# Performance work log

Hardware: AMD Instinct MI355X
Metric: run time of the kernel (lower is better)

Reference implementation:

```python
import jax, jax.numpy as jnp
import numpy as np

LN_EPS = 1e-5

def _layernorm(z, g, b):
    m = jnp.mean(z, axis=-1, keepdims=True)
    v = jnp.mean(jnp.square(z - m), axis=-1, keepdims=True)
    return (z - m) / jnp.sqrt(v + LN_EPS) * g + b

def setup_inputs() -> dict:
    key = jax.random.key(0)
    ks = jax.random.split(key, 8)
    B, N, C, H = 16, 1024, 384, 6
    Dff = 4 * C
    s = 0.02
    return {
        "x": jax.random.normal(ks[0], (B, N, C), dtype=jnp.float32),
        "ln1_g": jnp.ones((C,), jnp.float32),
        "ln1_b": jnp.zeros((C,), jnp.float32),
        "qkv_w": jax.random.normal(ks[1], (3 * C, C), jnp.float32) * s,
        "proj_w": jax.random.normal(ks[2], (C, C), jnp.float32) * s,
        "proj_b": jnp.zeros((C,), jnp.float32),
        "gate_h": jnp.ones((H,), jnp.float32),
        "ln2_g": jnp.ones((C,), jnp.float32),
        "ln2_b": jnp.zeros((C,), jnp.float32),
        "fc1_w": jax.random.normal(ks[3], (Dff, C), jnp.float32) * s,
        "fc1_b": jnp.zeros((Dff,), jnp.float32),
        "fc2_w": jax.random.normal(ks[4], (C, Dff), jnp.float32) * s,
        "fc2_b": jnp.zeros((C,), jnp.float32),
        "gate_mlp": jnp.ones((Dff,), jnp.float32),
    }

def reference(x, ln1_g, ln1_b, qkv_w, proj_w, proj_b, gate_h,
              ln2_g, ln2_b, fc1_w, fc1_b, fc2_w, fc2_b, gate_mlp):
    B, N, C = x.shape
    H = gate_h.shape[0]
    Dh = C // H
    scale = Dh ** -0.5

    # Attention branch
    h = _layernorm(x, ln1_g, ln1_b)
    qkv = (h @ qkv_w.T).reshape(B, N, 3, H, Dh).transpose(2, 0, 3, 1, 4)  # [3,B,H,N,Dh]
    q, k, v = qkv[0], qkv[1], qkv[2]
    attn = jax.nn.softmax(jnp.einsum('bhnd,bhmd->bhnm', q, k) * scale, axis=-1)  # [B,H,N,N]
    o = jnp.einsum('bhnm,bhmd->bhnd', attn, v)            # [B,H,N,Dh]
    o = o.transpose(0, 2, 1, 3) * gate_h[None, None, :, None]  # per-head gate
    o = o.reshape(B, N, C) @ proj_w.T + proj_b
    x = x + o

    # MLP branch (exact GELU, per-neuron gate)
    h2 = _layernorm(x, ln2_g, ln2_b)
    m = jax.nn.gelu(h2 @ fc1_w.T + fc1_b, approximate=False) * gate_mlp
    x = x + (m @ fc2_w.T + fc2_b)
    return x
```

## Files before the change

kernel.cpp:

```cpp
#include <hip/hip_runtime.h>
#include <hip/hip_bf16.h>
#include <cstdint>
#include <cstddef>

#define B_   16
#define N_   1024
#define C_   384
#define H_   6
#define DFF_ 1536
#define R_   16384

typedef __attribute__((ext_vector_type(8))) __bf16 bf16x8;
typedef __attribute__((ext_vector_type(4))) float  f32x4;
typedef __attribute__((ext_vector_type(8))) unsigned short u16x8;
typedef __attribute__((ext_vector_type(4))) unsigned short u16x4;

__device__ __forceinline__ float bf2f(unsigned short u){
    unsigned int x = ((unsigned int)u) << 16;
    return __builtin_bit_cast(float, x);
}
__device__ __forceinline__ unsigned short f2bf(float f){
    return __builtin_bit_cast(unsigned short, __float2bfloat16(f));
}
__device__ __forceinline__ unsigned int cvt_pk_bf16(float a, float b){
    unsigned int r;
    asm("v_cvt_pk_bf16_f32 %0, %1, %2" : "=v"(r) : "v"(a), "v"(b));
    return r;
}
__device__ __forceinline__ float fast_exp2(float x){
    float r;
    asm("v_exp_f32 %0, %1" : "=v"(r) : "v"(x));
    return r;
}
__device__ __forceinline__ void gload16(const void* g, void* l){
    __builtin_amdgcn_global_load_lds(
        (const __attribute__((address_space(1))) unsigned int*)g,
        (__attribute__((address_space(3))) unsigned int*)l, 16, 0, 0);
}
__device__ __forceinline__ float gelu_f(float u){
    float z  = fabsf(u) * 0.70710678118654752f;
    float t  = __builtin_amdgcn_rcpf(1.0f + 0.47047f*z);
    float e  = __expf(-z*z);
    float p  = t*(0.3480242f + t*(-0.0958798f + t*0.7478556f));
    float er = 1.0f - p*e;
    return 0.5f*u*(1.0f + copysignf(er, u));
}
__device__ __forceinline__ float ldv(const float* p, size_t i){ return p[i]; }
__device__ __forceinline__ float ldv(const __hip_bfloat16* p, size_t i){ return __bfloat162float(p[i]); }

__global__ __launch_bounds__(256) void ln1_cvt_kernel(
    const float* __restrict__ x, const float* __restrict__ g,
    const float* __restrict__ b, __hip_bfloat16* __restrict__ out,
    const float* __restrict__ i0, __hip_bfloat16* __restrict__ o0, int n0,
    const float* __restrict__ i1, __hip_bfloat16* __restrict__ o1, int n1,
    const float* __restrict__ i2, __hip_bfloat16* __restrict__ o2, int n2,
    const float* __restrict__ i3, __hip_bfloat16* __restrict__ o3, int n3)
{
    if (blockIdx.x < 4096){
        const int lane = threadIdx.x & 63;
        const int wave = threadIdx.x >> 6;
        const int row  = blockIdx.x*4 + wave;
        const float* xr = x + (size_t)row*C_;
        float v[6];
        float s = 0.f;
        #pragma unroll
        for (int i=0;i<6;i++){ v[i] = xr[lane + i*64]; s += v[i]; }
        #pragma unroll
        for (int m=1;m<64;m<<=1) s += __shfl_xor(s, m);
        const float mean = s * (1.0f/C_);
        float sq = 0.f;
        #pragma unroll
        for (int i=0;i<6;i++){ float d = v[i]-mean; sq += d*d; }
        #pragma unroll
        for (int m=1;m<64;m<<=1) sq += __shfl_xor(sq, m);
        const float rstd = rsqrtf(sq*(1.0f/C_) + 1e-5f);
        #pragma unroll
        for (int i=0;i<6;i++){
            int c = lane + i*64;
            out[(size_t)row*C_ + c] = __float2bfloat16((v[i]-mean)*rstd*g[c] + b[c]);
        }
    } else {
        const int total = n0+n1+n2+n3;
        for (int i = (blockIdx.x-4096)*blockDim.x + threadIdx.x; i < total; i += 1024*blockDim.x){
            int k = i;
            if (k < n0){ o0[k] = __float2bfloat16(i0[k]); continue; }
            k -= n0;
            if (k < n1){ o1[k] = __float2bfloat16(i1[k]); continue; }
            k -= n1;
            if (k < n2){ o2[k] = __float2bfloat16(i2[k]); continue; }
            k -= n2;
            o3[k] = __float2bfloat16(i3[k]);
        }
    }
}

template<typename T>
__global__ __launch_bounds__(256) void ln_kernel(
    const T* __restrict__ x, const float* __restrict__ g,
    const float* __restrict__ b, __hip_bfloat16* __restrict__ out)
{
    const int lane = threadIdx.x & 63;
    const int wave = threadIdx.x >> 6;
    const int row  = blockIdx.x*4 + wave;
    const T* xr = x + (size_t)row*C_;
    float v[6];
    float s = 0.f;
    #pragma unroll
    for (int i=0;i<6;i++){ v[i] = ldv(xr, lane + i*64); s += v[i]; }
    #pragma unroll
    for (int m=1;m<64;m<<=1) s += __shfl_xor(s, m);
    const float mean = s * (1.0f/C_);
    float sq = 0.f;
    #pragma unroll
    for (int i=0;i<6;i++){ float d = v[i]-mean; sq += d*d; }
    #pragma unroll
    for (int m=1;m<64;m<<=1) sq += __shfl_xor(sq, m);
    const float rstd = rsqrtf(sq*(1.0f/C_) + 1e-5f);
    #pragma unroll
    for (int i=0;i<6;i++){
        int c = lane + i*64;
        out[(size_t)row*C_ + c] = __float2bfloat16((v[i]-mean)*rstd*g[c] + b[c]);
    }
}

#define BK2 32
enum { EPI_QKV=0, EPI_PROJ=1, EPI_FC1=2, EPI_FC2=3 };

template<int EPI, int BMt, int BNt, int NBUF, int MW, int NTH>
__global__ __launch_bounds__(NTH, MW) void gemm_bt(
    const __hip_bfloat16* __restrict__ A,
    const __hip_bfloat16* __restrict__ W,
    const int M, const int N, const int K,
    const float* __restrict__ bias,
    const float* __restrict__ resid,
    const __hip_bfloat16* __restrict__ residb,
    const float* __restrict__ gate,
    float* __restrict__ outf,
    __hip_bfloat16* __restrict__ outb)
{
    constexpr int NWAVE = NTH/64;
    constexpr int NWC   = (BNt >= 128) ? 2 : 1;
    constexpr int NWR   = NWAVE/NWC;
    constexpr int WRS   = BMt/NWR;
    constexpr int MI    = WRS/16;
    constexpr int APASS = (BMt*BK2*2)/(NTH*16);
    constexpr int BPASS = (BNt*BK2*2)/(NTH*16);
    constexpr int RPP   = NTH/4;
    __shared__ __align__(16) unsigned short As[NBUF][BMt*BK2];
    __shared__ __align__(16) unsigned short Bs[NBUF][BNt*BK2];
    const int t = threadIdx.x;
    const int l = t & 63;
    const int w = t >> 6;
    const int wr = (NWC==2) ? (w >> 1) : w;
    const int wc = (NWC==2) ? (w & 1)  : 0;
    const int nb = N / BNt;
    const int rbX = (M/BMt) >> 3;
    const int X  = blockIdx.x & 7;
    const int j8 = blockIdx.x >> 3;
    const int rb = X*rbX + j8 / nb;
    const int cb = j8 % nb;
    const int srow2 = t >> 2;
    const int sgcol = (((t&3) - ((t>>3)&3)) & 3) * 8;
    f32x4 acc[MI][4];
    #pragma unroll
    for (int i=0;i<MI;i++)
        #pragma unroll
        for (int jj=0;jj<4;jj++) acc[i][jj] = (f32x4){0.f,0.f,0.f,0.f};

    const size_t arow0 = (size_t)rb*BMt + srow2;
    const size_t brow0 = (size_t)cb*BNt + srow2;

    auto STAGE = [&](int buf, int k0){
        #pragma unroll
        for (int c=0;c<APASS;c++)
            gload16(A + (arow0 + c*RPP)*K + k0 + sgcol, (char*)&As[buf][0] + c*(NTH*16) + t*16);
        #pragma unroll
        for (int c=0;c<BPASS;c++)
            gload16(W + (brow0 + c*RPP)*K + k0 + sgcol, (char*)&Bs[buf][0] + c*(NTH*16) + t*16);
    };

    auto COMPUTE = [&](int buf){
        const char* as = (const char*)&As[buf][0];
        const char* bs = (const char*)&Bs[buf][0];
        bf16x8 af[MI], bw[4];
        #pragma unroll
        for (int i=0;i<MI;i++){
            const int r = wr*WRS + i*16 + (l&15);
            const int sl = ((l>>4) + ((r>>1)&3)) & 3;
            af[i] = *(const bf16x8*)(as + r*64 + sl*16);
        }
        #pragma unroll
        for (int i=0;i<4;i++){
            const int r = wc*64 + i*16 + (l&15);
            const int sl = ((l>>4) + ((r>>1)&3)) & 3;
            bw[i] = *(const bf16x8*)(bs + r*64 + sl*16);
        }
        #pragma unroll
        for (int mi=0;mi<MI;mi++)
            #pragma unroll
            for (int ni=0;ni<4;ni++)
                acc[mi][ni] = __builtin_amdgcn_mfma_f32_16x16x32_bf16(af[mi], bw[ni], acc[mi][ni], 0,0,0);
    };

    const int nst = K/BK2;
    if constexpr (NBUF==2){
        STAGE(0, 0);
        for (int s=0; s<nst; ++s){
            asm volatile("s_waitcnt vmcnt(0)" ::: "memory");
            __builtin_amdgcn_s_barrier();
            asm volatile("" ::: "memory");
            if (s+1 < nst) STAGE((s+1)&1, (s+1)*BK2);
            COMPUTE(s&1);
        }
    } else {
        STAGE(0, 0);
        STAGE(1, BK2);
        int cur = 0, stb = 2;
        for (int s=0; s<nst; ++s){
            if (s < nst-1){
                if constexpr (APASS+BPASS==4) asm volatile("s_waitcnt vmcnt(4)" ::: "memory");
                else                          asm volatile("s_waitcnt vmcnt(3)" ::: "memory");
            } else {
                asm volatile("s_waitcnt vmcnt(0)" ::: "memory");
            }
            __builtin_amdgcn_s_barrier();
            asm volatile("" ::: "memory");
            if (s+2 < nst){
                STAGE(stb, (s+2)*BK2);
                stb = (stb+1==3) ? 0 : stb+1;
            }
            COMPUTE(cur);
            cur = (cur+1==3) ? 0 : cur+1;
        }
    }
    const int rowBase = rb*BMt + wr*WRS;
    const int colBase = cb*BNt + wc*64;
    if constexpr (EPI==EPI_QKV){
        unsigned short* ob = (unsigned short*)outb;
        #pragma unroll
        for (int ni=0; ni<4; ni++){
            const int col = colBase + ni*16 + (l&15);
            const int p = col/384, rem = col - p*384;
            const int hh = rem>>6, d = rem&63;
            #pragma unroll
            for (int mi=0; mi<MI; mi++){
                const int row0 = rowBase + mi*16 + (l>>4)*4;
                const int bb = row0>>10, n = row0&1023;
                if (p==2){
                    u16x4 pk;
                    #pragma unroll
                    for (int jj=0;jj<4;jj++) pk[jj] = f2bf(acc[mi][ni][jj]);
                    *(u16x4*)(ob + (size_t)2*6291456 + ((size_t)(bb*H_+hh)*64 + d)*1024 + n) = pk;
                } else {
                    #pragma unroll
                    for (int jj=0;jj<4;jj++)
                        ob[(((size_t)((p*16+bb)*6+hh))<<16) + ((size_t)(n+jj)<<6) + d] = f2bf(acc[mi][ni][jj]);
                }
            }
        }
    } else {
        #pragma unroll
        for (int ni=0; ni<4; ni++){
            const int col = colBase + ni*16 + (l&15);
            #pragma unroll
            for (int mi=0; mi<MI; mi++){
                #pragma unroll
                for (int jj=0;jj<4;jj++){
                    const int row = rowBase + mi*16 + (l>>4)*4 + jj;
                    const float vx = acc[mi][ni][jj];
                    size_t idx = (size_t)row*N + col;
                    if constexpr (EPI==EPI_PROJ){
                        outb[idx] = __float2bfloat16(resid[idx] + vx + bias[col]);
                    } else if constexpr (EPI==EPI_FC2){
                        outf[idx] = bf2f(*((const unsigned short*)residb + idx)) + vx + bias[col];
                    } else {
                        outb[idx] = __float2bfloat16(gelu_f(vx + bias[col]) * gate[col]);
                    }
                }
            }
        }
    }
}

__global__ __launch_bounds__(256) void attn_mfma(
    const __hip_bfloat16* __restrict__ qg,
    const __hip_bfloat16* __restrict__ kg,
    const __hip_bfloat16* __restrict__ vtg,
    const float* __restrict__ gate_h,
    __hip_bfloat16* __restrict__ og)
{
    __shared__ __align__(16) unsigned short Ks [3][64*64];
    __shared__ __align__(16) unsigned short Vts[3][64*64];
    const int t = threadIdx.x;
    const int l = t & 63;
    const int w = t >> 6;
    const int X  = blockIdx.x & 7;
    const int j8 = blockIdx.x >> 3;
    const int bh = X*12 + (j8 >> 3);
    const int n0 = (j8 & 7) * 128;
    const int h  = bh % H_;
    const int b  = bh / H_;
    const unsigned short* qp  = (const unsigned short*)qg  + ((size_t)bh*N_ + n0 + w*32)*64;
    const unsigned short* kp  = (const unsigned short*)kg  + (size_t)bh*N_*64;
    const unsigned short* vtp = (const unsigned short*)vtg + (size_t)bh*64*N_;

    bf16x8 qf[2][2];
    #pragma unroll
    for (int mt=0;mt<2;mt++)
        #pragma unroll
        for (int dc=0;dc<2;dc++){
            u16x8 raw = *(const u16x8*)(qp + ((size_t)(mt*16 + (l&15)))*64 + dc*32 + (l>>4)*8);
            u16x8 sc;
            #pragma unroll
            for (int j=0;j<8;j++) sc[j] = f2bf(bf2f(raw[j]) * 0.1803368801111244f);
            qf[mt][dc] = __builtin_bit_cast(bf16x8, sc);
        }

    int qk_off[4][2], pv_off[2][4];
    #pragma unroll
    for (int t4=0;t4<4;t4++){
        const int i    = l & 15;
        const int row  = 8*(i>>2) + (i&3) + 4*(t4&1) + 32*(t4>>1);
        const int swzr = (row&3) | (((row>>3)&1)<<2);
        #pragma unroll
        for (int dc=0;dc<2;dc++)
            qk_off[t4][dc] = row*128 + ((dc*64 + (l>>4)*16) ^ (swzr<<4));
    }
    #pragma unroll
    for (int nt=0;nt<4;nt++){
        const int row  = nt*16 + (l&15);
        const int swzr = (row&3) | (((row>>3)&1)<<2);
        #pragma unroll
        for (int kc=0;kc<2;kc++)
            pv_off[kc][nt] = row*128 + ((kc*64 + (l>>4)*16) ^ (swzr<<4));
    }

    const int sr  = t >> 3;
    const int sce = (t & 7) * 8;

    auto STAGE = [&](int buf, int kt){
        #pragma unroll
        for (int c=0;c<2;c++){
            const int r    = sr + c*32;
            const int swzr = (r&3) | (((r>>3)&1)<<2);
            const int col  = sce ^ (swzr<<3);
            gload16(kp  + ((size_t)(kt*64 + r))*64 + col, (char*)&Ks [buf][0] + (c*256 + t)*16);
            gload16(vtp + (size_t)r*N_ + kt*64 + col,     (char*)&Vts[buf][0] + (c*256 + t)*16);
        }
    };

    f32x4 o_acc[2][4];
    #pragma unroll
    for (int i=0;i<2;i++)
        #pragma unroll
        for (int jj=0;jj<4;jj++) o_acc[i][jj] = (f32x4){0.f,0.f,0.f,0.f};
    float rs_part[2] = {0.f, 0.f};

    STAGE(0, 0);
    STAGE(1, 1);
    int cur = 0, stb = 2;
    for (int kt=0; kt<16; kt++){
        if (kt < 15) asm volatile("s_waitcnt vmcnt(4)" ::: "memory");
        else         asm volatile("s_waitcnt vmcnt(0)" ::: "memory");
        __builtin_amdgcn_s_barrier();
        asm volatile("" ::: "memory");
        if (kt < 14){
            STAGE(stb, kt+2);
            stb = (stb+1==3) ? 0 : stb+1;
        }
        const char* ks = (const char*)&Ks[cur][0];
        const char* vs = (const char*)&Vts[cur][0];

        f32x4 s_acc[4][2];
        #pragma unroll
        for (int i=0;i<4;i++)
            #pragma unroll
            for (int jj=0;jj<2;jj++) s_acc[i][jj] = (f32x4){0.f,0.f,0.f,0.f};
        #pragma unroll
        for (int t4=0;t4<4;t4++)
            #pragma unroll
            for (int dc=0;dc<2;dc++){
                bf16x8 kf = *(const bf16x8*)(ks + qk_off[t4][dc]);
                #pragma unroll
                for (int mt=0;mt<2;mt++)
                    s_acc[t4][mt] = __builtin_amdgcn_mfma_f32_16x16x32_bf16(kf, qf[mt][dc], s_acc[t4][mt], 0,0,0);
            }
        #pragma unroll
        for (int mt=0;mt<2;mt++){
            float acc_s = 0.f;
            #pragma unroll
            for (int t4=0;t4<4;t4++){
                #pragma unroll
                for (int jj=0;jj<4;jj++){
                    float e = fast_exp2(s_acc[t4][mt][jj]);
                    s_acc[t4][mt][jj] = e;
                    acc_s += e;
                }
            }
            rs_part[mt] += acc_s;
        }
        #pragma unroll
        for (int kc=0;kc<2;kc++){
            union { unsigned int u[4]; bf16x8 v; } pu[2];
            #pragma unroll
            for (int mt=0;mt<2;mt++){
                pu[mt].u[0] = cvt_pk_bf16(s_acc[2*kc  ][mt][0], s_acc[2*kc  ][mt][1]);
                pu[mt].u[1] = cvt_pk_bf16(s_acc[2*kc  ][mt][2], s_acc[2*kc  ][mt][3]);
                pu[mt].u[2] = cvt_pk_bf16(s_acc[2*kc+1][mt][0], s_acc[2*kc+1][mt][1]);
                pu[mt].u[3] = cvt_pk_bf16(s_acc[2*kc+1][mt][2], s_acc[2*kc+1][mt][3]);
            }
            #pragma unroll
            for (int nt=0;nt<4;nt++){
                bf16x8 vf = *(const bf16x8*)(vs + pv_off[kc][nt]);
                #pragma unroll
                for (int mt=0;mt<2;mt++)
                    o_acc[mt][nt] = __builtin_amdgcn_mfma_f32_16x16x32_bf16(pu[mt].v, vf, o_acc[mt][nt], 0,0,0);
            }
        }
        cur = (cur+1==3) ? 0 : cur+1;
    }
    float rowsum[2];
    #pragma unroll
    for (int mt=0;mt<2;mt++){
        float rs = rs_part[mt];
        rs += __shfl_xor(rs, 16);
        rs += __shfl_xor(rs, 32);
        rowsum[mt] = rs;
    }
    const float gh = gate_h[h];
    float inv[2][4];
    #pragma unroll
    for (int mt=0;mt<2;mt++)
        #pragma unroll
        for (int r=0;r<4;r++)
            inv[mt][r] = gh / __shfl(rowsum[mt], (l>>4)*4 + r, 16);
    unsigned short* op = (unsigned short*)og + ((size_t)b*N_ + n0 + w*32)*C_ + h*64;
    #pragma unroll
    for (int mt=0;mt<2;mt++){
        #pragma unroll
        for (int r=0;r<4;r++){
            const int n = mt*16 + (l>>4)*4 + r;
            #pragma unroll
            for (int nt=0;nt<4;nt++)
                op[(size_t)n*C_ + nt*16 + (l&15)] = f2bf(o_acc[mt][nt][r]*inv[mt][r]);
        }
    }
}

extern "C" void kernel_launch(void* const* d_in, const int* in_sizes, int n_in,
                              void* d_out, int out_size, void* d_ws, size_t ws_size,
                              hipStream_t stream)
{
    const float* x     = (const float*)d_in[0];
    const float* ln1g  = (const float*)d_in[1];
    const float* ln1b  = (const float*)d_in[2];
    const float* qkvw  = (const float*)d_in[3];
    const float* projw = (const float*)d_in[4];
    const float* projb = (const float*)d_in[5];
    const float* gateh = (const float*)d_in[6];
    const float* ln2g  = (const float*)d_in[7];
    const float* ln2b  = (const float*)d_in[8];
    const float* fc1w  = (const float*)d_in[9];
    const float* fc1b  = (const float*)d_in[10];
    const float* fc2w  = (const float*)d_in[11];
    const float* fc2b  = (const float*)d_in[12];
    const float* gatem = (const float*)d_in[13];
    float* out = (float*)d_out;

    char* ws = (char*)d_ws;
    __hip_bfloat16* h_buf = (__hip_bfloat16*)(ws + 0);
    __hip_bfloat16* qkv   = (__hip_bfloat16*)(ws + 12582912);
    __hip_bfloat16* q_buf = qkv;
    __hip_bfloat16* k_buf = qkv + 6291456;
    __hip_bfloat16* vt_buf= qkv + 2*6291456;
    __hip_bfloat16* o_buf = (__hip_bfloat16*)(ws + 50331648);
    __hip_bfloat16* m_buf = (__hip_bfloat16*)(ws + 12582912);
    __hip_bfloat16* x1b   = (__hip_bfloat16*)(ws + 62914560);
    __hip_bfloat16* wqkv  = (__hip_bfloat16*)(ws + 88080384);
    __hip_bfloat16* wproj = (__hip_bfloat16*)(ws + 88965120);
    __hip_bfloat16* wfc1  = (__hip_bfloat16*)(ws + 89260032);
    __hip_bfloat16* wfc2  = (__hip_bfloat16*)(ws + 90439680);

    ln1_cvt_kernel<<<5120, 256, 0, stream>>>(x, ln1g, ln1b, h_buf,
                                             qkvw, wqkv, 1152*384,
                                             projw, wproj, 384*384,
                                             fc1w, wfc1, 1536*384,
                                             fc2w, wfc2, 384*1536);

    gemm_bt<EPI_QKV,128,64,3,4,256><<<2304, 256, 0, stream>>>(h_buf, wqkv, R_, 1152, 384,
                                                              nullptr, nullptr, nullptr, nullptr, nullptr, qkv);
    attn_mfma<<<768, 256, 0, stream>>>(q_buf, k_buf, vt_buf, gateh, o_buf);
    gemm_bt<EPI_PROJ,64,128,3,1,256><<<768, 256, 0, stream>>>(o_buf, wproj, R_, 384, 384,
                                                              projb, x, nullptr, nullptr, nullptr, x1b);
    ln_kernel<__hip_bfloat16><<<4096, 256, 0, stream>>>(x1b, ln2g, ln2b, h_buf);
    gemm_bt<EPI_FC1,128,64,3,4,256><<<3072, 256, 0, stream>>>(h_buf, wfc1, R_, 1536, 384,
                                                              fc1b, nullptr, nullptr, gatem, nullptr, m_buf);
    gemm_bt<EPI_FC2,64,128,3,1,256><<<768, 256, 0, stream>>>(m_buf, wfc2, R_, 384, 1536,
                                                             fc2b, nullptr, x1b, nullptr, out, nullptr);
}
```

Before: 186.5 us.

## Add weight-resident FC1 GEMM kernel and widen QKV GEMM tile

Adds a dedicated FC1 GEMM kernel that loads the block's full 64x384 weight slice into shared memory once. Only 128-row activation tiles are streamed through a 3-deep buffer, with the GELU and gate epilogue fused in. The QKV GEMM also moves to a 128x128 tile with fewer blocks and a different occupancy hint. The aim is to cut repeated weight staging and barrier overhead, at the cost of about 48KB of weight LDS per block, which may limit occupancy.

```diff
diff --git a/kernel.cpp b/kernel.cpp
--- a/kernel.cpp
+++ b/kernel.cpp
@@ -145,6 +145,7 @@
     constexpr int MI    = WRS/16;
     constexpr int APASS = (BMt*BK2*2)/(NTH*16);
     constexpr int BPASS = (BNt*BK2*2)/(NTH*16);
+    constexpr int LPT   = APASS + BPASS;
     constexpr int RPP   = NTH/4;
     __shared__ __align__(16) unsigned short As[NBUF][BMt*BK2];
     __shared__ __align__(16) unsigned short Bs[NBUF][BNt*BK2];
@@ -218,8 +219,8 @@
         int cur = 0, stb = 2;
         for (int s=0; s<nst; ++s){
             if (s < nst-1){
-                if constexpr (APASS+BPASS==4) asm volatile("s_waitcnt vmcnt(4)" ::: "memory");
-                else                          asm volatile("s_waitcnt vmcnt(3)" ::: "memory");
+                if constexpr (LPT==4) asm volatile("s_waitcnt vmcnt(4)" ::: "memory");
+                else                  asm volatile("s_waitcnt vmcnt(3)" ::: "memory");
             } else {
                 asm volatile("s_waitcnt vmcnt(0)" ::: "memory");
             }
@@ -277,6 +278,95 @@
                         outb[idx] = __float2bfloat16(gelu_f(vx + bias[col]) * gate[col]);
                     }
                 }
+            }
+        }
+    }
+}
+
+__global__ __launch_bounds__(256, 2) void gemm_wres_fc1(
+    const __hip_bfloat16* __restrict__ A,
+    const __hip_bfloat16* __restrict__ Wt,
+    const float* __restrict__ bias,
+    const float* __restrict__ gate,
+    __hip_bfloat16* __restrict__ outb)
+{
+    __shared__ __align__(16) unsigned short As[3][128*32];
+    __shared__ __align__(16) unsigned short Bs[64*384];
+    const int t = threadIdx.x;
+    const int l = t & 63;
+    const int w = t >> 6;
+    const int nb = 24;
+    const int X  = blockIdx.x & 7;
+    const int j8 = blockIdx.x >> 3;
+    const int rb = X*16 + j8 / nb;
+    const int cb = j8 % nb;
+
+    #pragma unroll
+    for (int j=0;j<12;j++){
+        const int L   = (w*12 + j)*1024 + l*16;
+        const int row = L / 768;
+        const int cbyte = L - row*768;
+        const int scol  = (cbyte ^ ((row&7)<<4)) >> 1;
+        gload16(Wt + (size_t)(cb*64 + row)*384 + scol, (char*)&Bs[0] + L);
+    }
+    const int sgcol = (((l&3) - ((l>>3)&3)) & 3) * 8;
+    const size_t arowW = (size_t)rb*128 + w*32 + (l>>2);
+    auto STAGEA = [&](int buf, int s){
+        #pragma unroll
+        for (int c=0;c<2;c++)
+            gload16(A + (arowW + c*16)*384 + s*32 + sgcol,
+                    (char*)&As[buf][0] + w*2048 + c*1024 + l*16);
+    };
+    STAGEA(0, 0);
+    STAGEA(1, 1);
+    asm volatile("s_waitcnt vmcnt(4)" ::: "memory");
+    __builtin_amdgcn_s_barrier();
+
+    f32x4 acc[2][4];
+    #pragma unroll
+    for (int i=0;i<2;i++)
+        #pragma unroll
+        for (int jj=0;jj<4;jj++) acc[i][jj] = (f32x4){0.f,0.f,0.f,0.f};
+
+    const char* asbase = (const char*)&As[0][0];
+    #pragma unroll
+    for (int s=0; s<12; ++s){
+        if (s < 11) asm volatile("s_waitcnt vmcnt(2)" ::: "memory");
+        else        asm volatile("s_waitcnt vmcnt(0)" ::: "memory");
+        const char* as = asbase + (s%3)*8192 + w*2048;
+        bf16x8 af[2], bw[4];
+        #pragma unroll
+        for (int i=0;i<2;i++){
+            const int r  = i*16 + (l&15);
+            const int sl = ((l>>4) + ((r>>1)&3)) & 3;
+            af[i] = *(const bf16x8*)(as + r*64 + sl*16);
+        }
+        #pragma unroll
+        for (int i=0;i<4;i++){
+            const int r = i*16 + (l&15);
+            bw[i] = *(const bf16x8*)((const char*)&Bs[0] + r*768
+                         + ((s*64 + (l>>4)*16) ^ ((r&7)<<4)));
+        }
+        #pragma unroll
+        for (int mi=0;mi<2;mi++)
+            #pragma unroll
+            for (int ni=0;ni<4;ni++)
+                acc[mi][ni] = __builtin_amdgcn_mfma_f32_16x16x32_bf16(af[mi], bw[ni], acc[mi][ni], 0,0,0);
+        asm volatile("s_waitcnt lgkmcnt(0)" ::: "memory");
+        if (s+2 < 12) STAGEA((s+2)%3, s+2);
+    }
+    const int rowBase = rb*128 + w*32;
+    const int colBase = cb*64;
+    #pragma unroll
+    for (int ni=0; ni<4; ni++){
+        const int col = colBase + ni*16 + (l&15);
+        #pragma unroll
+        for (int mi=0; mi<2; mi++){
+            #pragma unroll
+            for (int jj=0;jj<4;jj++){
+                const int row = rowBase + mi*16 + (l>>4)*4 + jj;
+                outb[(size_t)row*1536 + col] =
+                    __float2bfloat16(gelu_f(acc[mi][ni][jj] + bias[col]) * gate[col]);
             }
         }
     }
@@ -487,14 +577,13 @@
                                              fc1w, wfc1, 1536*384,
                                              fc2w, wfc2, 384*1536);
 
-    gemm_bt<EPI_QKV,128,64,3,4,256><<<2304, 256, 0, stream>>>(h_buf, wqkv, R_, 1152, 384,
-                                                              nullptr, nullptr, nullptr, nullptr, nullptr, qkv);
+    gemm_bt<EPI_QKV,128,128,3,3,256><<<1152, 256, 0, stream>>>(h_buf, wqkv, R_, 1152, 384,
+                                                               nullptr, nullptr, nullptr, nullptr, nullptr, qkv);
     attn_mfma<<<768, 256, 0, stream>>>(q_buf, k_buf, vt_buf, gateh, o_buf);
     gemm_bt<EPI_PROJ,64,128,3,1,256><<<768, 256, 0, stream>>>(o_buf, wproj, R_, 384, 384,
                                                               projb, x, nullptr, nullptr, nullptr, x1b);
     ln_kernel<__hip_bfloat16><<<4096, 256, 0, stream>>>(x1b, ln2g, ln2b, h_buf);
-    gemm_bt<EPI_FC1,128,64,3,4,256><<<3072, 256, 0, stream>>>(h_buf, wfc1, R_, 1536, 384,
-                                                              fc1b, nullptr, nullptr, gatem, nullptr, m_buf);
+    gemm_wres_fc1<<<3072, 256, 0, stream>>>(h_buf, wfc1, fc1b, gatem, m_buf);
     gemm_bt<EPI_FC2,64,128,3,1,256><<<768, 256, 0, stream>>>(m_buf, wfc2, R_, 384, 1536,
                                                              fc2b, nullptr, x1b, nullptr, out, nullptr);
 }
```

New measurement: 177.9 us. 4.6% less time.
